# Kernel tuning notes

Hardware: AMD Instinct MI355X
Metric: run time of the kernel (lower is better)

Reference implementation:

```python
import jax, jax.numpy as jnp
import numpy as np
from jax import lax

ALPHA = 1.0
BETA = 2.0
NUM_ANTS = 16384
NUM_NODES = 512
BATCH = 4096


def setup_inputs() -> dict:
    key = jax.random.key(0)
    k1, k2, k3 = jax.random.split(key, 3)
    x = jax.random.normal(k1, (BATCH, NUM_NODES), dtype=jnp.float32)
    # matches nn.Parameter(torch.ones(N,N)*0.1)
    pheromone_trails = jnp.ones((NUM_NODES, NUM_NODES), dtype=jnp.float32) * 0.1
    # matches nn.Parameter(torch.rand(N,N)*0.1)
    heuristic_info = jax.random.uniform(k2, (NUM_NODES, NUM_NODES), dtype=jnp.float32) * 0.1
    # matches register_buffer('ant_positions', randint(0, N, (num_ants,)))
    ant_positions = jax.random.randint(k3, (NUM_ANTS,), 0, NUM_NODES, dtype=jnp.int32)
    return {"x": x, "pheromone_trails": pheromone_trails,
            "heuristic_info": heuristic_info, "ant_positions": ant_positions}


def reference(x, pheromone_trails, heuristic_info, ant_positions):
    A, N = NUM_ANTS, NUM_NODES
    ant_ids = jnp.arange(A)

    # NOTE: the torch code's select_next_node always reads the row of the ant's
    # *initial* position (self.ant_positions is never updated inside forward),
    # so the unmasked scores are constant per ant. We replicate that faithfully.
    base = (pheromone_trails[ant_positions] ** ALPHA) * \
           (heuristic_info[ant_positions] ** BETA)          # [A, N]

    visited0 = jnp.zeros((A, N), dtype=bool).at[ant_ids, ant_positions].set(True)
    plen0 = jnp.zeros((A,), dtype=jnp.float32)

    def step(carry, _):
        key, visited, current, plen = carry
        key, sub = jax.random.split(key)
        # torch sets masked entries to 0 (NOT -inf) before softmax; replicate.
        logits = jnp.where(visited, 0.0, base)               # [A, N]
        # categorical == multinomial(softmax(logits), 1), vectorized over ants
        nxt = jax.random.categorical(sub, logits, axis=-1)   # [A] int
        plen = plen + heuristic_info[current, nxt]
        visited = visited.at[ant_ids, nxt].set(True)
        return (key, visited, nxt, plen), nxt

    carry0 = (jax.random.key(42), visited0, ant_positions.astype(jnp.int32), plen0)
    (_, _, _, path_lengths), sampled = lax.scan(step, carry0, None, length=N - 1)

    # full paths: [A, N] = start node followed by N-1 sampled nodes
    paths = jnp.concatenate([ant_positions[:, None].astype(sampled.dtype),
                             sampled.T], axis=1)
    # sequential 'if path_length < best' with strict < keeps the FIRST minimum,
    # which is exactly jnp.argmin
    best_idx = jnp.argmin(path_lengths)
    best_path = paths[best_idx].astype(jnp.float32)          # [N]
    return jnp.broadcast_to(best_path[None, :], (x.shape[0], N))
```

## Files before the change

### kernel.cpp

```cpp
#include <hip/hip_runtime.h>
#include <cstdint>
#include <cstddef>

#define A_NUM_ANTS   16384
#define N_NODES      512
#define N_STEPS      511
#define N_BATCH      4096

constexpr uint32_t rotl32(uint32_t x, int r) { return (x << r) | (x >> (32 - r)); }

constexpr void tf2x32(uint32_t k0, uint32_t k1, uint32_t x0, uint32_t x1,
                      uint32_t& o0, uint32_t& o1) {
  const uint32_t k2 = k0 ^ k1 ^ 0x1BD11BDAu;
  x0 += k0; x1 += k1;
  x0 += x1; x1 = rotl32(x1, 13); x1 ^= x0;
  x0 += x1; x1 = rotl32(x1, 15); x1 ^= x0;
  x0 += x1; x1 = rotl32(x1, 26); x1 ^= x0;
  x0 += x1; x1 = rotl32(x1,  6); x1 ^= x0;
  x0 += k1; x1 += k2 + 1u;
  x0 += x1; x1 = rotl32(x1, 17); x1 ^= x0;
  x0 += x1; x1 = rotl32(x1, 29); x1 ^= x0;
  x0 += x1; x1 = rotl32(x1, 16); x1 ^= x0;
  x0 += x1; x1 = rotl32(x1, 24); x1 ^= x0;
  x0 += k2; x1 += k0 + 2u;
  x0 += x1; x1 = rotl32(x1, 13); x1 ^= x0;
  x0 += x1; x1 = rotl32(x1, 15); x1 ^= x0;
  x0 += x1; x1 = rotl32(x1, 26); x1 ^= x0;
  x0 += x1; x1 = rotl32(x1,  6); x1 ^= x0;
  x0 += k0; x1 += k1 + 3u;
  x0 += x1; x1 = rotl32(x1, 17); x1 ^= x0;
  x0 += x1; x1 = rotl32(x1, 29); x1 ^= x0;
  x0 += x1; x1 = rotl32(x1, 16); x1 ^= x0;
  x0 += x1; x1 = rotl32(x1, 24); x1 ^= x0;
  x0 += k1; x1 += k2 + 4u;
  x0 += x1; x1 = rotl32(x1, 13); x1 ^= x0;
  x0 += x1; x1 = rotl32(x1, 15); x1 ^= x0;
  x0 += x1; x1 = rotl32(x1, 26); x1 ^= x0;
  x0 += x1; x1 = rotl32(x1,  6); x1 ^= x0;
  x0 += k2; x1 += k0 + 5u;
  o0 = x0; o1 = x1;
}

struct Subkeys { uint32_t k0[N_STEPS]; uint32_t k1[N_STEPS]; };

constexpr Subkeys make_subkeys() {
  Subkeys s{};
  uint32_t c0 = 0u, c1 = 42u;
  for (int t = 0; t < N_STEPS; ++t) {
    uint32_t n0 = 0, n1 = 0, s0 = 0, s1 = 0;
    tf2x32(c0, c1, 0u, 0u, n0, n1);
    tf2x32(c0, c1, 0u, 1u, s0, s1);
    s.k0[t] = s0; s.k1[t] = s1;
    c0 = n0; c1 = n1;
  }
  return s;
}

namespace { constexpr Subkeys H_SUBKEYS = make_subkeys(); }
__device__ __constant__ Subkeys SUBKEYS = H_SUBKEYS;

#define NEG_LN2   (-0.69314718056f)

__device__ __forceinline__ uint32_t drotl(uint32_t x, int r) {
  return __builtin_rotateleft32(x, (uint32_t)r);
}

__device__ __forceinline__ uint32_t tf_hash(uint32_t k0, uint32_t k1,
                                            uint32_t k2, uint32_t x1i) {
  uint32_t x0 = k0, x1 = x1i;
#define TFR(r) { x0 += x1; x1 = drotl(x1, r); x1 ^= x0; }
  TFR(13) TFR(15) TFR(26) TFR(6)
  x0 += k1; x1 += k2 + 1u;
  TFR(17) TFR(29) TFR(16) TFR(24)
  x0 += k2; x1 += k0 + 2u;
  TFR(13) TFR(15) TFR(26) TFR(6)
  x0 += k0; x1 += k1 + 3u;
  TFR(17) TFR(29) TFR(16) TFR(24)
  x0 += k1; x1 += k2 + 4u;
  TFR(13) TFR(15) TFR(26) TFR(6)
  x0 += k2; x1 += k0 + 5u;
#undef TFR
  return x0 ^ x1;
}

__device__ __forceinline__ uint32_t umax(uint32_t a, uint32_t b) {
  return a > b ? a : b;
}

struct Frag { uint32_t m[8]; };

template <bool WRITE_PATH>
__device__ __forceinline__ void simulate_ant(
    int a, int lane,
    const float* __restrict__ pher,
    const float* __restrict__ heur,
    int pos,
    float* __restrict__ plen_out,
    float* __restrict__ path_out)
{
  a   = __builtin_amdgcn_readfirstlane(a);
  pos = __builtin_amdgcn_readfirstlane(pos);

  float lm[8];
  unsigned long long vq[8];
  float ebmin, ebmax;
  {
    const float* hrow = heur + (size_t)pos * N_NODES;
    const float* prow = pher + (size_t)pos * N_NODES;
    ebmin = 1.0f; ebmax = 1.0f;
#pragma unroll
    for (int q = 0; q < 8; ++q) {
      const int n = lane * 8 + q;
      const float hv = hrow[n];
      const float base = prow[n] * (hv * hv);
      const float eb = expf(-base);
      lm[q] = NEG_LN2 * eb;
      ebmin = fminf(ebmin, eb);
      ebmax = fmaxf(ebmax, eb);
      vq[q] = 0ull;
    }
    vq[pos & 7] = 1ull << (pos >> 3);
  }

  int baddr[6];
#pragma unroll
  for (int r = 0; r < 6; ++r) {
    baddr[r] = ((lane ^ (1 << r)) << 2);
    asm volatile("" : "+v"(baddr[r]));
  }

#pragma unroll
  for (int r = 0; r < 6; ++r) {
    ebmin = fminf(ebmin, __int_as_float(
        __builtin_amdgcn_ds_bpermute(baddr[r], __float_as_int(ebmin))));
    ebmax = fmaxf(ebmax, __int_as_float(
        __builtin_amdgcn_ds_bpermute(baddr[r], __float_as_int(ebmax))));
  }
  ebmin = __int_as_float(__builtin_amdgcn_readfirstlane(__float_as_int(ebmin)));
  ebmax = __int_as_float(__builtin_amdgcn_readfirstlane(__float_as_int(ebmax)));
  const float ratio = ebmax / ebmin;
  const float delta = ratio * (1.0f + 3e-4f) - 1.0f + 1e-5f;
  const float d15   = delta * 1.5f;
  const bool  always_slow = !(d15 < 0.4f);
  const uint32_t D32 = always_slow ? 0xFFFFFFFFu
                     : ((uint32_t)(d15 * 4294967296.0f) + 1u);

  int   cur  = pos;
  float plen = 0.0f;
  if (WRITE_PATH && lane == 0) path_out[0] = (float)pos;

  const uint32_t ctr_base = (uint32_t)(a * N_NODES + lane * 8);

  auto hash8 = [&](Frag& f, int t) __attribute__((always_inline)) {
    const uint32_t k0 = SUBKEYS.k0[t];
    const uint32_t k1 = SUBKEYS.k1[t];
    const uint32_t k2 = k0 ^ k1 ^ 0x1BD11BDAu;
#pragma unroll
    for (int q = 0; q < 8; ++q)
      f.m[q] = tf_hash(k0, k1, k2, ctr_base + (k1 + (uint32_t)q));
  };

  auto step = [&](Frag& use, Frag& pre, int t, int tpre, bool do_pre)
      __attribute__((always_inline)) {
    const uint32_t t0 = umax(umax(use.m[0], use.m[1]), use.m[2]);
    const uint32_t t1 = umax(umax(use.m[3], use.m[4]), use.m[5]);
    const uint32_t t2 = umax(umax(use.m[6], use.m[7]), t0);
    uint32_t xmax = umax(t1, t2);
#pragma unroll
    for (int r = 0; r < 6; ++r) {
      const uint32_t o = (uint32_t)__builtin_amdgcn_ds_bpermute(baddr[r], (int)xmax);
      xmax = umax(xmax, o);
    }

    if (do_pre) hash8(pre, tpre);

    const uint32_t xmax_s = (uint32_t)__builtin_amdgcn_readfirstlane((int)xmax);
    const uint32_t mmax_s = xmax_s >> 9;
    const uint32_t d   = 8388608u - mmax_s;
    const uint32_t sub = __umulhi(D32, d) + 2u;
    const uint32_t thr32 = (mmax_s - sub) << 9;
    const bool force_slow = always_slow || (mmax_s < 4194304u);

    unsigned long long b[8];
    int tot = 0;
#pragma unroll
    for (int q = 0; q < 8; ++q) {
      b[q] = __ballot(use.m[q] >= thr32);
      tot += __popcll(b[q]);
    }

    int bn;
    if (!force_slow && tot == 1) {
      bn = 0;
#pragma unroll
      for (int q = 0; q < 8; ++q)
        if (b[q]) bn = (int)__builtin_ctzll(b[q]) * 8 + q;
    } else {
      float s[8];
#pragma unroll
      for (int q = 0; q < 8; ++q) {
        const uint32_t m  = use.m[q] >> 9;
        const float f  = __uint_as_float(m | 0x3f800000u) - 1.0f;
        const float le = ((vq[q] >> lane) & 1ull) ? NEG_LN2 : lm[q];
        s[q] = __log2f(f) * le;
      }
      float smin = s[0];
#pragma unroll
      for (int q = 1; q < 8; ++q) smin = fminf(smin, s[q]);
#pragma unroll
      for (int r = 0; r < 6; ++r)
        smin = fminf(smin, __int_as_float(
            __builtin_amdgcn_ds_bpermute(baddr[r], __float_as_int(smin))));
      int fq = 8;
#pragma unroll
      for (int q = 7; q >= 0; --q) if (s[q] == smin) fq = q;
      const unsigned long long mask = __ballot(fq < 8);
      const int winlane = __builtin_ctzll(mask);
      bn = __builtin_amdgcn_readfirstlane(__shfl(fq, winlane, 64)) + winlane * 8;
    }

    {
      const unsigned long long nb = 1ull << (bn >> 3);
      const int qq = bn & 7;
#pragma unroll
      for (int q = 0; q < 8; ++q) vq[q] |= (qq == q) ? nb : 0ull;
    }

    plen += heur[(size_t)cur * N_NODES + bn];
    cur = bn;
    if (WRITE_PATH && lane == 0) path_out[t + 1] = (float)bn;
  };

  Frag A, B;
  hash8(A, 0);
  for (int tt = 0; tt < (N_STEPS - 1) / 2; ++tt) {
    const int t0 = 2 * tt;
    step(A, B, t0,     t0 + 1, true);
    step(B, A, t0 + 1, t0 + 2, true);
  }
  step(A, B, N_STEPS - 1, 0, false);

  if (!WRITE_PATH && lane == 0) plen_out[a] = plen;
}

__global__ __launch_bounds__(256, 6) void aco_sim_kernel(
    const float* __restrict__ pher, const float* __restrict__ heur,
    const int* __restrict__ pos0, float* __restrict__ plen_out, int num_ants)
{
  const int a = (int)((blockIdx.x * blockDim.x + threadIdx.x) >> 6);
  const int lane = threadIdx.x & 63;
  if (a >= num_ants) return;
  simulate_ant<false>(a, lane, pher, heur, pos0[a], plen_out, nullptr);
}

__global__ void aco_argmin_kernel(const float* __restrict__ plen,
                                  int* __restrict__ best, int num_ants) {
  const int tid = threadIdx.x;
  float bv = 3.4e38f;
  int   bi = 0;
  bool  have = false;
  for (int i = tid; i < num_ants; i += 256) {
    const float v = plen[i];
    if (!have || v < bv) { bv = v; bi = i; have = true; }
  }
#pragma unroll
  for (int off = 32; off >= 1; off >>= 1) {
    const float vo = __shfl_xor(bv, off, 64);
    const int   io = __shfl_xor(bi, off, 64);
    if (vo < bv || (vo == bv && io < bi)) { bv = vo; bi = io; }
  }
  __shared__ float sv[4];
  __shared__ int   si[4];
  const int w = tid >> 6;
  if ((tid & 63) == 0) { sv[w] = bv; si[w] = bi; }
  __syncthreads();
  if (tid == 0) {
    for (int j = 1; j < 4; ++j)
      if (sv[j] < bv || (sv[j] == bv && si[j] < bi)) { bv = sv[j]; bi = si[j]; }
    bi = bi < 0 ? 0 : (bi >= num_ants ? num_ants - 1 : bi);
    *best = bi;
  }
}

__global__ void aco_resim_kernel(const float* __restrict__ pher,
                                 const float* __restrict__ heur,
                                 const int* __restrict__ pos0,
                                 const int* __restrict__ best,
                                 float* __restrict__ path_out, int num_ants) {
  const int lane = threadIdx.x & 63;
  int a = *best;
  a = a < 0 ? 0 : (a >= num_ants ? num_ants - 1 : a);
  simulate_ant<true>(a, lane, pher, heur, pos0[a], nullptr, path_out);
}

__global__ void aco_bcast_kernel(float* __restrict__ out, int total4) {
  const int j = (int)(blockIdx.x * blockDim.x + threadIdx.x);
  if (j >= total4) return;
  const int row  = 1 + (j >> 7);
  const int col4 = j & 127;
  const float4 v = reinterpret_cast<const float4*>(out)[col4];
  reinterpret_cast<float4*>(out)[row * 128 + col4] = v;
}

extern "C" void kernel_launch(void* const* d_in, const int* in_sizes, int n_in,
                              void* d_out, int out_size, void* d_ws, size_t ws_size,
                              hipStream_t stream) {
  const float* pher = (const float*)d_in[1];
  const float* heur = (const float*)d_in[2];
  const int*   pos  = (const int*)d_in[3];
  float* out = (float*)d_out;
  const int num_ants = in_sizes[3];

  float* plen = out;
  int*   best = (int*)(out + A_NUM_ANTS);

  const int sim_blocks = (num_ants * 64 + 255) / 256;
  aco_sim_kernel<<<dim3(sim_blocks), dim3(256), 0, stream>>>(
      pher, heur, pos, plen, num_ants);
  aco_argmin_kernel<<<dim3(1), dim3(256), 0, stream>>>(plen, best, num_ants);
  aco_resim_kernel<<<dim3(1), dim3(64), 0, stream>>>(
      pher, heur, pos, best, out, num_ants);
  const int total4 = (out_size - N_NODES) / 4;
  aco_bcast_kernel<<<dim3((total4 + 255) / 256), dim3(256), 0, stream>>>(
      out, total4);
}
```

Before: 8.396 ms.

## Use DPP wave max reduction, per-lane visited bitmask, and precomputed k2 subkeys

Replaces the ds_bpermute butterfly max-reduction on the per-step hot path with DPP row shifts/broadcasts and reads the result from lane 63. Visited state becomes an 8-bit per-lane mask instead of eight 64-bit wave-uniform masks, cutting register pressure and per-step update work. The k2 subkey is precomputed into constant memory and the counter base add is hoisted. The remaining reductions switch to __shfl_xor, which may compile to similar ds instructions.

```diff
diff --git a/kernel.cpp b/kernel.cpp
--- a/kernel.cpp
+++ b/kernel.cpp
@@ -41,7 +41,7 @@
   o0 = x0; o1 = x1;
 }
 
-struct Subkeys { uint32_t k0[N_STEPS]; uint32_t k1[N_STEPS]; };
+struct Subkeys { uint32_t k0[N_STEPS]; uint32_t k1[N_STEPS]; uint32_t k2[N_STEPS]; };
 
 constexpr Subkeys make_subkeys() {
   Subkeys s{};
@@ -50,7 +50,7 @@
     uint32_t n0 = 0, n1 = 0, s0 = 0, s1 = 0;
     tf2x32(c0, c1, 0u, 0u, n0, n1);
     tf2x32(c0, c1, 0u, 1u, s0, s1);
-    s.k0[t] = s0; s.k1[t] = s1;
+    s.k0[t] = s0; s.k1[t] = s1; s.k2[t] = s0 ^ s1 ^ 0x1BD11BDAu;
     c0 = n0; c1 = n1;
   }
   return s;
@@ -87,6 +87,16 @@
   return a > b ? a : b;
 }
 
+__device__ __forceinline__ uint32_t wave_umax_dpp(uint32_t x) {
+  x = umax(x, (uint32_t)__builtin_amdgcn_update_dpp(0, (int)x, 0x111, 0xf, 0xf, false));
+  x = umax(x, (uint32_t)__builtin_amdgcn_update_dpp(0, (int)x, 0x112, 0xf, 0xf, false));
+  x = umax(x, (uint32_t)__builtin_amdgcn_update_dpp(0, (int)x, 0x114, 0xf, 0xf, false));
+  x = umax(x, (uint32_t)__builtin_amdgcn_update_dpp(0, (int)x, 0x118, 0xf, 0xf, false));
+  x = umax(x, (uint32_t)__builtin_amdgcn_update_dpp(0, (int)x, 0x142, 0xf, 0xf, false));
+  x = umax(x, (uint32_t)__builtin_amdgcn_update_dpp(0, (int)x, 0x143, 0xf, 0xf, false));
+  return x;
+}
+
 struct Frag { uint32_t m[8]; };
 
 template <bool WRITE_PATH>
@@ -101,9 +111,9 @@
   a   = __builtin_amdgcn_readfirstlane(a);
   pos = __builtin_amdgcn_readfirstlane(pos);
 
-  float lm[8];
-  unsigned long long vq[8];
-  float ebmin, ebmax;
+  float    lm[8];
+  uint32_t visited = 0;
+  float    ebmin, ebmax;
   {
     const float* hrow = heur + (size_t)pos * N_NODES;
     const float* prow = pher + (size_t)pos * N_NODES;
@@ -117,24 +127,14 @@
       lm[q] = NEG_LN2 * eb;
       ebmin = fminf(ebmin, eb);
       ebmax = fmaxf(ebmax, eb);
-      vq[q] = 0ull;
+      if (n == pos) visited |= (1u << q);
     }
-    vq[pos & 7] = 1ull << (pos >> 3);
-  }
-
-  int baddr[6];
-#pragma unroll
-  for (int r = 0; r < 6; ++r) {
-    baddr[r] = ((lane ^ (1 << r)) << 2);
-    asm volatile("" : "+v"(baddr[r]));
-  }
-
-#pragma unroll
-  for (int r = 0; r < 6; ++r) {
-    ebmin = fminf(ebmin, __int_as_float(
-        __builtin_amdgcn_ds_bpermute(baddr[r], __float_as_int(ebmin))));
-    ebmax = fmaxf(ebmax, __int_as_float(
-        __builtin_amdgcn_ds_bpermute(baddr[r], __float_as_int(ebmax))));
+  }
+
+#pragma unroll
+  for (int off = 1; off < 64; off <<= 1) {
+    ebmin = fminf(ebmin, __shfl_xor(ebmin, off, 64));
+    ebmax = fmaxf(ebmax, __shfl_xor(ebmax, off, 64));
   }
   ebmin = __int_as_float(__builtin_amdgcn_readfirstlane(__float_as_int(ebmin)));
   ebmax = __int_as_float(__builtin_amdgcn_readfirstlane(__float_as_int(ebmax)));
@@ -154,10 +154,11 @@
   auto hash8 = [&](Frag& f, int t) __attribute__((always_inline)) {
     const uint32_t k0 = SUBKEYS.k0[t];
     const uint32_t k1 = SUBKEYS.k1[t];
-    const uint32_t k2 = k0 ^ k1 ^ 0x1BD11BDAu;
+    const uint32_t k2 = SUBKEYS.k2[t];
+    const uint32_t xb = ctr_base + k1;
 #pragma unroll
     for (int q = 0; q < 8; ++q)
-      f.m[q] = tf_hash(k0, k1, k2, ctr_base + (k1 + (uint32_t)q));
+      f.m[q] = tf_hash(k0, k1, k2, xb + (uint32_t)q);
   };
 
   auto step = [&](Frag& use, Frag& pre, int t, int tpre, bool do_pre)
@@ -165,16 +166,11 @@
     const uint32_t t0 = umax(umax(use.m[0], use.m[1]), use.m[2]);
     const uint32_t t1 = umax(umax(use.m[3], use.m[4]), use.m[5]);
     const uint32_t t2 = umax(umax(use.m[6], use.m[7]), t0);
-    uint32_t xmax = umax(t1, t2);
-#pragma unroll
-    for (int r = 0; r < 6; ++r) {
-      const uint32_t o = (uint32_t)__builtin_amdgcn_ds_bpermute(baddr[r], (int)xmax);
-      xmax = umax(xmax, o);
-    }
+    const uint32_t xmax = wave_umax_dpp(umax(t1, t2));
 
     if (do_pre) hash8(pre, tpre);
 
-    const uint32_t xmax_s = (uint32_t)__builtin_amdgcn_readfirstlane((int)xmax);
+    const uint32_t xmax_s = (uint32_t)__builtin_amdgcn_readlane((int)xmax, 63);
     const uint32_t mmax_s = xmax_s >> 9;
     const uint32_t d   = 8388608u - mmax_s;
     const uint32_t sub = __umulhi(D32, d) + 2u;
@@ -201,16 +197,15 @@
       for (int q = 0; q < 8; ++q) {
         const uint32_t m  = use.m[q] >> 9;
         const float f  = __uint_as_float(m | 0x3f800000u) - 1.0f;
-        const float le = ((vq[q] >> lane) & 1ull) ? NEG_LN2 : lm[q];
+        const float le = ((visited >> q) & 1u) ? NEG_LN2 : lm[q];
         s[q] = __log2f(f) * le;
       }
       float smin = s[0];
 #pragma unroll
       for (int q = 1; q < 8; ++q) smin = fminf(smin, s[q]);
 #pragma unroll
-      for (int r = 0; r < 6; ++r)
-        smin = fminf(smin, __int_as_float(
-            __builtin_amdgcn_ds_bpermute(baddr[r], __float_as_int(smin))));
+      for (int off = 1; off < 64; off <<= 1)
+        smin = fminf(smin, __shfl_xor(smin, off, 64));
       int fq = 8;
 #pragma unroll
       for (int q = 7; q >= 0; --q) if (s[q] == smin) fq = q;
@@ -219,12 +214,7 @@
       bn = __builtin_amdgcn_readfirstlane(__shfl(fq, winlane, 64)) + winlane * 8;
     }
 
-    {
-      const unsigned long long nb = 1ull << (bn >> 3);
-      const int qq = bn & 7;
-#pragma unroll
-      for (int q = 0; q < 8; ++q) vq[q] |= (qq == q) ? nb : 0ull;
-    }
+    if ((bn >> 3) == lane) visited |= (1u << (bn & 7));
 
     plen += heur[(size_t)cur * N_NODES + bn];
     cur = bn;
```

After: 8.009 ms. 4.6% less time.
